# Optimization experiments

Measured on AMD Instinct MI355X. Metric: run time of the kernel, lower is better.

Reference implementation:

```python
import jax, jax.numpy as jnp
import numpy as np

B = 2097152  # batch
H = 2        # GRU hidden size


def _gru_cell(x, h, w_ih, w_hh, b_ih, b_hh):
    # torch.nn.GRUCell math. w_ih: [3H, I], w_hh: [3H, H]
    gi = x @ w_ih.T + b_ih  # [B, 3H]
    gh = h @ w_hh.T + b_hh  # [B, 3H]
    i_r, i_z, i_n = jnp.split(gi, 3, axis=-1)
    h_r, h_z, h_n = jnp.split(gh, 3, axis=-1)
    r = jax.nn.sigmoid(i_r + h_r)
    z = jax.nn.sigmoid(i_z + h_z)
    n = jnp.tanh(i_n + r * h_n)
    return (1.0 - z) * n + z * h


def setup_inputs() -> dict:
    key = jax.random.key(0)
    ks = jax.random.split(key, 14)
    f32 = jnp.float32
    inp = {
        "x": jax.random.normal(ks[0], (B, 18), dtype=f32),
        # r_up: GRUCell(2, 2)
        "w_ih_up": 0.3 * jax.random.normal(ks[1], (3 * H, 2), dtype=f32),
        "w_hh_up": 0.3 * jax.random.normal(ks[2], (3 * H, H), dtype=f32),
        "b_ih_up": 0.1 * jax.random.normal(ks[3], (3 * H,), dtype=f32),
        "b_hh_up": 0.1 * jax.random.normal(ks[4], (3 * H,), dtype=f32),
        # fc_obs: Linear(6, 2)
        "w_obs": 0.3 * jax.random.normal(ks[5], (2, 6), dtype=f32),
        "b_obs": 0.1 * jax.random.normal(ks[6], (2,), dtype=f32),
        # r_down: GRUCell(2, 2)
        "w_ih_dn": 0.3 * jax.random.normal(ks[7], (3 * H, 2), dtype=f32),
        "w_hh_dn": 0.3 * jax.random.normal(ks[8], (3 * H, H), dtype=f32),
        "b_ih_dn": 0.1 * jax.random.normal(ks[9], (3 * H,), dtype=f32),
        "b_hh_dn": 0.1 * jax.random.normal(ks[10], (3 * H,), dtype=f32),
        # fc_out: Linear(2, 1)
        "w_out": 0.3 * jax.random.normal(ks[11], (1, H), dtype=f32),
        "b_out": 0.1 * jax.random.normal(ks[12], (1,), dtype=f32),
    }
    return inp


def reference(x, w_ih_up, w_hh_up, b_ih_up, b_hh_up, w_obs, b_obs,
              w_ih_dn, w_hh_dn, b_ih_dn, b_hh_dn, w_out, b_out):
    obs = x[:, :4]            # [B, 4]
    j = x[:, 4:11]            # [B, 7]
    jd = x[:, 11:]            # [B, 7]
    jcat = jnp.stack([j, jd], axis=1)  # [B, 2, 7]

    # upward recurrence over the 7 joints, reversed order
    h = jnp.zeros((x.shape[0], H), dtype=x.dtype)
    h_up = []
    for i in reversed(range(7)):
        h = _gru_cell(jcat[:, :, i], h, w_ih_up, w_hh_up, b_ih_up, b_hh_up)
        h_up.append(h)

    # fuse observation into the hidden state
    h = jnp.concatenate([obs, h], axis=1) @ w_obs.T + b_obs  # [B, 2]

    # downward recurrence, emitting one action per joint
    acts = []
    for i in range(7):
        h = _gru_cell(h_up[i], h, w_ih_dn, w_hh_dn, b_ih_dn, b_hh_dn)
        acts.append(h @ w_out.T + b_out)  # [B, 1]
    return jnp.concatenate(acts, axis=1)  # [B, 7]
```

## Files before the change

kernel.cpp:

```cpp
#include <hip/hip_runtime.h>


using v2f = __attribute__((ext_vector_type(2))) float;

__device__ __forceinline__ float fexp2(float x) { return __builtin_amdgcn_exp2f(x); }
__device__ __forceinline__ float frcp(float x)  { return __builtin_amdgcn_rcpf(x); }

struct Cell {
    v2f wr0, wr1, ur0, ur1, br;
    v2f wz0, wz1, uz0, uz1, bz;
    v2f wn0, wn1, bni;
    v2f un0, un1, bnh;
};

__global__ void prep_kernel(
    const float* __restrict__ w_ih_up, const float* __restrict__ w_hh_up,
    const float* __restrict__ b_ih_up, const float* __restrict__ b_hh_up,
    const float* __restrict__ w_obs,   const float* __restrict__ b_obs,
    const float* __restrict__ w_ih_dn, const float* __restrict__ w_hh_dn,
    const float* __restrict__ b_ih_dn, const float* __restrict__ b_hh_dn,
    const float* __restrict__ w_out,   const float* __restrict__ b_out,
    float* __restrict__ ws)
{
    if (threadIdx.x != 0 || blockIdx.x != 0) return;
    const float s1 = -1.4426950408889634f;
    const float s2 =  2.8853900817779268f;
    #pragma unroll
    for (int c = 0; c < 2; ++c) {
        const float* wi = c ? w_ih_dn : w_ih_up;
        const float* wh = c ? w_hh_dn : w_hh_up;
        const float* bi = c ? b_ih_dn : b_ih_up;
        const float* bh = c ? b_hh_dn : b_hh_up;
        float* o = ws + c * 64;
        o[0] = s1*wi[0]; o[1] = s1*wi[2];  o[2] = s1*wi[1]; o[3] = s1*wi[3];
        o[4] = s1*wh[0]; o[5] = s1*wh[2];  o[6] = s1*wh[1]; o[7] = s1*wh[3];
        o[8] = s1*(bi[0]+bh[0]); o[9] = s1*(bi[1]+bh[1]);
        o[10] = s1*wi[4]; o[11] = s1*wi[6]; o[12] = s1*wi[5]; o[13] = s1*wi[7];
        o[14] = s1*wh[4]; o[15] = s1*wh[6]; o[16] = s1*wh[5]; o[17] = s1*wh[7];
        o[18] = s1*(bi[2]+bh[2]); o[19] = s1*(bi[3]+bh[3]);
        o[20] = s2*wi[8]; o[21] = s2*wi[10]; o[22] = s2*wi[9]; o[23] = s2*wi[11];
        o[24] = s2*bi[4]; o[25] = s2*bi[5];
        o[26] = s2*wh[8]; o[27] = s2*wh[10]; o[28] = s2*wh[9]; o[29] = s2*wh[11];
        o[30] = s2*bh[4]; o[31] = s2*bh[5];
    }
    #pragma unroll
    for (int i = 0; i < 12; ++i) ws[128 + i] = w_obs[i];
    ws[140] = b_obs[0]; ws[141] = b_obs[1];
    ws[142] = w_out[0]; ws[143] = w_out[1];
    ws[144] = b_out[0];
}

__device__ __forceinline__ void gru(const Cell& c, float x0, float x1, v2f& h) {
    v2f gr = c.br + c.wr0 * x0 + c.wr1 * x1 + c.ur0 * h.x + c.ur1 * h.y;
    v2f gz = c.bz + c.wz0 * x0 + c.wz1 * x1 + c.uz0 * h.x + c.uz1 * h.y;
    v2f dr = (v2f){1.0f + fexp2(gr.x), 1.0f + fexp2(gr.y)};
    v2f dz = (v2f){1.0f + fexp2(gz.x), 1.0f + fexp2(gz.y)};
    float invr = frcp(dr.x * dr.y);
    v2f r = invr * (v2f){dr.y, dr.x};
    v2f gi = c.bni + c.wn0 * x0 + c.wn1 * x1;
    v2f gh = c.bnh + c.un0 * h.x + c.un1 * h.y;
    v2f a  = gi + r * gh;
    v2f da = (v2f){1.0f + fexp2(a.x), 1.0f + fexp2(a.y)};
    float m = -2.0f * frcp(da.x * da.y);
    v2f n = (v2f){fmaf(m, da.y, 1.0f), fmaf(m, da.x, 1.0f)};
    float invz = frcp(dz.x * dz.y);
    v2f z = invz * (v2f){dz.y, dz.x};
    h = n + z * (h - n);
}

__device__ __forceinline__ void row_chain(
    const Cell& up, const Cell& dn, const float* __restrict__ W,
    const float* row, float acts[7])
{
    v2f h = (v2f){0.0f, 0.0f};
    v2f hu[7];
    #pragma unroll
    for (int k = 0; k < 7; ++k) {
        const int i = 6 - k;
        gru(up, row[4 + i], row[11 + i], h);
        hu[k] = h;
    }
    {
        v2f t = (v2f){W[140], W[141]};
        #pragma unroll
        for (int c = 0; c < 4; ++c)
            t += (v2f){W[128 + c], W[134 + c]} * row[c];
        t += (v2f){W[132], W[138]} * h.x;
        t += (v2f){W[133], W[139]} * h.y;
        h = t;
    }
    const float wo0 = W[142], wo1 = W[143], bo = W[144];
    #pragma unroll
    for (int k = 0; k < 7; ++k) {
        gru(dn, hu[k].x, hu[k].y, h);
        acts[k] = fmaf(wo0, h.x, fmaf(wo1, h.y, bo));
    }
}

__global__ __launch_bounds__(256) void recpolicy_kernel(
    const float* __restrict__ x, const float* __restrict__ W,
    float* __restrict__ out, int n)
{
    __shared__ float lds[4608];
    const int tid  = threadIdx.x;
    const int wid  = tid >> 6;
    const int lane = tid & 63;
    const int rowbase = blockIdx.x * 256 + wid * 64;
    float* wlds = lds + wid * 1152;

    const Cell up = *reinterpret_cast<const Cell*>(W);
    const Cell dn = *reinterpret_cast<const Cell*>(W + 64);

    if (rowbase + 64 <= n) {
        const float4* src = reinterpret_cast<const float4*>(x + (size_t)rowbase * 18);
        float4* dst = reinterpret_cast<float4*>(wlds);
        #pragma unroll
        for (int k = 0; k < 4; ++k)
            dst[lane + k * 64] = src[lane + k * 64];
        if (lane < 32) dst[lane + 256] = src[lane + 256];

        const float* row = wlds + lane * 18;
        float acts[7];
        row_chain(up, dn, W, row, acts);

        #pragma unroll
        for (int k = 0; k < 7; ++k) wlds[lane * 7 + k] = acts[k];

        const float4* so = reinterpret_cast<const float4*>(wlds);
        float4* dsto = reinterpret_cast<float4*>(out + (size_t)rowbase * 7);
        dsto[lane] = so[lane];
        if (lane < 48) dsto[lane + 64] = so[lane + 64];
    } else if (rowbase < n) {
        const int rg = rowbase + lane;
        if (rg < n) {
            float rowl[18];
            #pragma unroll
            for (int i = 0; i < 18; ++i) rowl[i] = x[(size_t)rg * 18 + i];
            float acts[7];
            row_chain(up, dn, W, rowl, acts);
            #pragma unroll
            for (int k = 0; k < 7; ++k) out[(size_t)rg * 7 + k] = acts[k];
        }
    }
}

extern "C" void kernel_launch(void* const* d_in, const int* in_sizes, int n_in,
                              void* d_out, int out_size, void* d_ws, size_t ws_size,
                              hipStream_t stream) {
    const float* x       = (const float*)d_in[0];
    const float* w_ih_up = (const float*)d_in[1];
    const float* w_hh_up = (const float*)d_in[2];
    const float* b_ih_up = (const float*)d_in[3];
    const float* b_hh_up = (const float*)d_in[4];
    const float* w_obs   = (const float*)d_in[5];
    const float* b_obs   = (const float*)d_in[6];
    const float* w_ih_dn = (const float*)d_in[7];
    const float* w_hh_dn = (const float*)d_in[8];
    const float* b_ih_dn = (const float*)d_in[9];
    const float* b_hh_dn = (const float*)d_in[10];
    const float* w_out   = (const float*)d_in[11];
    const float* b_out   = (const float*)d_in[12];
    float* out = (float*)d_out;
    float* ws  = (float*)d_ws;

    prep_kernel<<<1, 64, 0, stream>>>(
        w_ih_up, w_hh_up, b_ih_up, b_hh_up, w_obs, b_obs,
        w_ih_dn, w_hh_dn, b_ih_dn, b_hh_dn, w_out, b_out, ws);

    const int n = in_sizes[0] / 18;
    const int block = 256;
    const int grid = (n + block - 1) / block;
    recpolicy_kernel<<<grid, block, 0, stream>>>(x, ws, out, n);
}
```

Baseline: 52.54 us.

## Use persistent grid-stride waves with register prefetch of next tile

Replaces the one-tile-per-wave launch with a fixed grid of 2048 blocks in which each wave loops over 64-row tiles. While it computes the current tile, it prefetches the next tile's input into registers, so global load latency overlaps the GRU arithmetic. This removes per-block launch and prologue cost (including reloading the weight struct). The trade-offs are higher register pressure from the five prefetched float4 values and possible load imbalance across waves.

```diff
diff --git a/kernel.cpp b/kernel.cpp
--- a/kernel.cpp
+++ b/kernel.cpp
@@ -105,33 +105,62 @@
     const int tid  = threadIdx.x;
     const int wid  = tid >> 6;
     const int lane = tid & 63;
-    const int rowbase = blockIdx.x * 256 + wid * 64;
     float* wlds = lds + wid * 1152;
 
     const Cell up = *reinterpret_cast<const Cell*>(W);
     const Cell dn = *reinterpret_cast<const Cell*>(W + 64);
 
-    if (rowbase + 64 <= n) {
-        const float4* src = reinterpret_cast<const float4*>(x + (size_t)rowbase * 18);
-        float4* dst = reinterpret_cast<float4*>(wlds);
-        #pragma unroll
-        for (int k = 0; k < 4; ++k)
-            dst[lane + k * 64] = src[lane + k * 64];
-        if (lane < 32) dst[lane + 256] = src[lane + 256];
-
-        const float* row = wlds + lane * 18;
-        float acts[7];
-        row_chain(up, dn, W, row, acts);
-
-        #pragma unroll
-        for (int k = 0; k < 7; ++k) wlds[lane * 7 + k] = acts[k];
-
-        const float4* so = reinterpret_cast<const float4*>(wlds);
-        float4* dsto = reinterpret_cast<float4*>(out + (size_t)rowbase * 7);
-        dsto[lane] = so[lane];
-        if (lane < 48) dsto[lane + 64] = so[lane + 64];
-    } else if (rowbase < n) {
-        const int rg = rowbase + lane;
+    const int NT = n >> 6;
+    const int NW = gridDim.x << 2;
+    const int gw = (blockIdx.x << 2) | wid;
+
+    const float4* xs = reinterpret_cast<const float4*>(x);
+
+    int t = gw;
+    if (t < NT) {
+        float4 nx0, nx1, nx2, nx3, nx4;
+        {
+            size_t b = (size_t)t * 288;
+            nx0 = xs[b + lane];       nx1 = xs[b + 64 + lane];
+            nx2 = xs[b + 128 + lane]; nx3 = xs[b + 192 + lane];
+            if (lane < 32) nx4 = xs[b + 256 + lane];
+        }
+        while (true) {
+            {
+                float4* d = reinterpret_cast<float4*>(wlds);
+                d[lane] = nx0;       d[lane + 64]  = nx1;
+                d[lane + 128] = nx2; d[lane + 192] = nx3;
+                if (lane < 32) d[lane + 256] = nx4;
+            }
+            const int tn = t + NW;
+            if (tn < NT) {
+                size_t b = (size_t)tn * 288;
+                nx0 = xs[b + lane];       nx1 = xs[b + 64 + lane];
+                nx2 = xs[b + 128 + lane]; nx3 = xs[b + 192 + lane];
+                if (lane < 32) nx4 = xs[b + 256 + lane];
+            }
+
+            const float* row = wlds + lane * 18;
+            float acts[7];
+            row_chain(up, dn, W, row, acts);
+
+            #pragma unroll
+            for (int k = 0; k < 7; ++k) wlds[lane * 7 + k] = acts[k];
+            {
+                const float4* so = reinterpret_cast<const float4*>(wlds);
+                float4* dsto = reinterpret_cast<float4*>(out) + (size_t)t * 112;
+                dsto[lane] = so[lane];
+                if (lane < 48) dsto[lane + 64] = so[lane + 64];
+            }
+
+            if (tn >= NT) break;
+            t = tn;
+        }
+    }
+
+    const int tail0 = NT << 6;
+    if (gw == 0 && tail0 < n) {
+        const int rg = tail0 + lane;
         if (rg < n) {
             float rowl[18];
             #pragma unroll
@@ -168,7 +197,5 @@
         w_ih_dn, w_hh_dn, b_ih_dn, b_hh_dn, w_out, b_out, ws);
 
     const int n = in_sizes[0] / 18;
-    const int block = 256;
-    const int grid = (n + block - 1) / block;
-    recpolicy_kernel<<<grid, block, 0, stream>>>(x, ws, out, n);
-}
+    recpolicy_kernel<<<2048, 256, 0, stream>>>(x, ws, out, n);
+}
```

Result: slower. 53.63 us (+2.1%).
